# Kernel optimization log

Hardware: AMD Instinct MI355X
Metric: run time of the kernel (lower is better)

## Reference

```python
import jax, jax.numpy as jnp
import numpy as np

D = 2048      # model dim
H = 16        # query heads
KV = 4        # kv heads (GQA)
HD = 128      # head dim
L = 128       # latent dim (must equal HD for the residual add in the original module)
B = 2
S = 2048
ROPE_THETA = 10000.0


def _rope_cos_sin(seq_len, hd, start_pos, dtype):
    inv_freq = 1.0 / (ROPE_THETA ** (jnp.arange(0, hd, 2, dtype=jnp.float32) / hd))
    pos = jnp.arange(seq_len, dtype=jnp.float32) + start_pos
    freqs = pos[:, None] * inv_freq[None, :]          # [S, HD/2]
    emb = jnp.concatenate([freqs, freqs], axis=-1)    # [S, HD]
    return jnp.cos(emb).astype(dtype), jnp.sin(emb).astype(dtype)


def _rotate_half(x):
    h = x.shape[-1] // 2
    return jnp.concatenate([-x[..., h:], x[..., :h]], axis=-1)


def setup_inputs() -> dict:
    key = jax.random.key(0)
    ks = jax.random.split(key, 8)
    std = D ** -0.5
    x = jax.random.normal(ks[0], (B, S, D), dtype=jnp.float32)
    # causal mask [B, 1, S, S], 1 = keep, 0 = masked
    causal = jnp.tril(jnp.ones((S, S), dtype=jnp.int32))
    mask = jnp.broadcast_to(causal[None, None], (B, 1, S, S))
    # weights stored as [in, out] (== torch Linear weight transposed)
    wq = jax.random.normal(ks[1], (D, H * HD), dtype=jnp.float32) * std
    wk = jax.random.normal(ks[2], (D, KV * HD), dtype=jnp.float32) * std
    wv = jax.random.normal(ks[3], (D, KV * HD), dtype=jnp.float32) * std
    w_ql = jax.random.normal(ks[4], (D, L), dtype=jnp.float32) * std
    w_kl = jax.random.normal(ks[5], (D, L), dtype=jnp.float32) * std
    wo = jax.random.normal(ks[6], (H * HD, D), dtype=jnp.float32) * std
    return {"x": x, "mask": mask, "wq": wq, "wk": wk, "wv": wv,
            "w_ql": w_ql, "w_kl": w_kl, "wo": wo, "start_pos": 0}


def reference(x, mask, wq, wk, wv, w_ql, w_kl, wo, start_pos):
    b, s, _ = x.shape
    q = (x @ wq).reshape(b, s, H, HD)
    k = (x @ wk).reshape(b, s, KV, HD)
    v = (x @ wv).reshape(b, s, KV, HD)
    q_latent = x @ w_ql                               # [B,S,L]
    kv_latent = x @ w_kl                              # [B,S,L]

    cos, sin = _rope_cos_sin(s, HD, start_pos, x.dtype)
    c = cos[None, :, None, :]
    sn = sin[None, :, None, :]
    q = q * c + _rotate_half(q) * sn
    k = k * c + _rotate_half(k) * sn

    q = q.transpose(0, 2, 1, 3)                       # [B,H,S,HD]
    k = k.transpose(0, 2, 1, 3)                       # [B,KV,S,HD]
    v = v.transpose(0, 2, 1, 3)
    rep = H // KV
    k = jnp.repeat(k, rep, axis=1)                    # GQA repeat_interleave -> [B,H,S,HD]
    v = jnp.repeat(v, rep, axis=1)

    scores = jnp.einsum('bhqd,bhkd->bhqk', q, k) * (HD ** -0.5)
    scores = jnp.where(mask == 0, -jnp.inf, scores)
    attn = jax.nn.softmax(scores, axis=-1)
    out = jnp.einsum('bhqk,bhkd->bhqd', attn, v)
    out = out.transpose(0, 2, 1, 3).reshape(b, s, H * HD)

    latent_scores = jnp.einsum('bqd,bkd->bqk', q_latent, kv_latent) * (L ** -0.5)
    latent_scores = jnp.where(jnp.squeeze(mask, axis=1) == 0, -jnp.inf, latent_scores)
    latent_w = jax.nn.softmax(latent_scores, axis=-1)
    latent_out = jnp.einsum('bqk,bkd->bqd', latent_w, kv_latent)   # [B,S,L]

    # faithful to torch: unsqueeze(1).expand(B,H,S,L).contiguous().view(B,S,H*L)
    latent_exp = jnp.broadcast_to(latent_out[:, None], (b, H, s, L)).reshape(b, s, H * L)
    combined = out + latent_exp
    return combined @ wo
```

## Files before the change

kernel.cpp:

```cpp
#include <hip/hip_runtime.h>
#include <hip/hip_bf16.h>

typedef __bf16 bf16x8 __attribute__((ext_vector_type(8)));
typedef float f32x4 __attribute__((ext_vector_type(4)));
typedef unsigned short u16;

__device__ __forceinline__ float b2f(u16 u) {
  union { unsigned int i; float f; } v; v.i = ((unsigned int)u) << 16; return v.f;
}
__device__ __forceinline__ u16 f2b(float f) {
  union { float f; unsigned int i; } v; v.f = f;
  unsigned int r = v.i + 0x7fffu + ((v.i >> 16) & 1u);
  return (u16)(r >> 16);
}
__device__ __forceinline__ void gld_lds16(const u16* g, u16* l) {
  __builtin_amdgcn_global_load_lds(
      (const __attribute__((address_space(1))) unsigned int*)g,
      (__attribute__((address_space(3))) unsigned int*)l, 16, 0, 0);
}

#define NPROJ 3328

__global__ __launch_bounds__(256) void cvt_x(const float* __restrict__ x, u16* __restrict__ xb) {
  int i = (blockIdx.x * 256 + threadIdx.x) * 4;
  float4 v = *(const float4*)(x + i);
  u16 o[4] = { f2b(v.x), f2b(v.y), f2b(v.z), f2b(v.w) };
  *(uint2*)(xb + i) = *(uint2*)o;
}

__global__ __launch_bounds__(256) void prep_wt1(
    const float* __restrict__ wq, const float* __restrict__ wk, const float* __restrict__ wv,
    const float* __restrict__ wql, const float* __restrict__ wkl, u16* __restrict__ wt1) {
  __shared__ u16 lds[64][80];
  int bn = blockIdx.x % 52, bk = blockIdx.x / 52;
  int n0 = bn * 64, k0 = bk * 64;
  const float* src; int srcN, c0;
  if (n0 < 2048)      { src = wq;  srcN = 2048; c0 = n0; }
  else if (n0 < 2560) { src = wk;  srcN = 512;  c0 = n0 - 2048; }
  else if (n0 < 3072) { src = wv;  srcN = 512;  c0 = n0 - 2560; }
  else if (n0 < 3200) { src = wql; srcN = 128;  c0 = n0 - 3072; }
  else                { src = wkl; srcN = 128;  c0 = n0 - 3200; }
  int t = threadIdx.x;
  int row = t >> 2, cg = (t & 3) * 16;
  const float* p = src + (size_t)(k0 + row) * srcN + c0 + cg;
  u16 tmp[16];
#pragma unroll
  for (int g = 0; g < 4; ++g) {
    float4 v = *(const float4*)(p + g * 4);
    tmp[g*4+0] = f2b(v.x); tmp[g*4+1] = f2b(v.y);
    tmp[g*4+2] = f2b(v.z); tmp[g*4+3] = f2b(v.w);
  }
  *(uint4*)&lds[row][cg]     = *(uint4*)&tmp[0];
  *(uint4*)&lds[row][cg + 8] = *(uint4*)&tmp[8];
  __syncthreads();
  int n = t >> 2, kg = (t & 3) * 16;
  u16 ov[16];
#pragma unroll
  for (int i = 0; i < 16; ++i) ov[i] = lds[kg + i][n];
  u16* dst = wt1 + (size_t)(n0 + n) * 2048 + k0 + kg;
  *(uint4*)&dst[0] = *(uint4*)&ov[0];
  *(uint4*)&dst[8] = *(uint4*)&ov[8];
}

__global__ __launch_bounds__(256) void prep_wt2(const float* __restrict__ wo, u16* __restrict__ wt2) {
  __shared__ u16 lds[64][80];
  int bn = blockIdx.x & 31, bk = blockIdx.x >> 5;
  int n0 = bn * 64, k0 = bk * 64;
  int t = threadIdx.x;
  int row = t >> 2, cg = (t & 3) * 16;
  const float* p = wo + (size_t)(k0 + row) * 2048 + n0 + cg;
  u16 tmp[16];
#pragma unroll
  for (int g = 0; g < 4; ++g) {
    float4 v = *(const float4*)(p + g * 4);
    tmp[g*4+0] = f2b(v.x); tmp[g*4+1] = f2b(v.y);
    tmp[g*4+2] = f2b(v.z); tmp[g*4+3] = f2b(v.w);
  }
  *(uint4*)&lds[row][cg]     = *(uint4*)&tmp[0];
  *(uint4*)&lds[row][cg + 8] = *(uint4*)&tmp[8];
  __syncthreads();
  int n = t >> 2, kg = (t & 3) * 16;
  u16 ov[16];
#pragma unroll
  for (int i = 0; i < 16; ++i) ov[i] = lds[kg + i][n];
  u16* dst = wt2 + (size_t)(n0 + n) * 2048 + k0 + kg;
  *(uint4*)&dst[0] = *(uint4*)&ov[0];
  *(uint4*)&dst[8] = *(uint4*)&ov[8];
}

__global__ __launch_bounds__(256) void rope_table(float2* __restrict__ cs) {
  int idx = blockIdx.x * 256 + threadIdx.x;
  int p = idx >> 6, i = idx & 63;
  float invf = exp2f(-(float)i * 0.20762050593046938f);
  float a = (float)p * invf;
  cs[idx] = make_float2(cosf(a), sinf(a));
}

__global__ __launch_bounds__(256) void gemm_bf16(
    const u16* __restrict__ A, const u16* __restrict__ Bt, u16* __restrict__ C,
    float* __restrict__ Cf,
    int K, int lda, int ldb, int ldc, int nbn, const u16* __restrict__ lat) {
  __shared__ u16 As[128 * 64];
  __shared__ u16 Bs[128 * 64];
  int bm = blockIdx.x / nbn, bn = blockIdx.x % nbn;
  int m0 = bm * 128, n0 = bn * 128;
  int t = threadIdx.x;
  int lane = t & 63, wave = t >> 6;
  int wm = (wave >> 1) * 64, wn = (wave & 1) * 64;
  int lr = lane & 15, lg = lane >> 4;
  f32x4 acc[4][4] = {};
  for (int kt = 0; kt < K; kt += 64) {
    __syncthreads();
#pragma unroll
    for (int p = 0; p < 4; ++p) {
      int c = (p * 4 + wave) * 64 + lane;
      int row = c >> 3, col = (c & 7) * 8;
      gld_lds16(A + (size_t)(m0 + row) * lda + kt + col, As + c * 8);
      gld_lds16(Bt + (size_t)(n0 + row) * ldb + kt + col, Bs + c * 8);
    }
    __syncthreads();
#pragma unroll
    for (int ks = 0; ks < 2; ++ks) {
      bf16x8 af[4], bj[4];
#pragma unroll
      for (int i = 0; i < 4; ++i)
        af[i] = *(const bf16x8*)(As + (wm + i * 16 + lr) * 64 + ks * 32 + lg * 8);
#pragma unroll
      for (int j = 0; j < 4; ++j)
        bj[j] = *(const bf16x8*)(Bs + (wn + j * 16 + lr) * 64 + ks * 32 + lg * 8);
#pragma unroll
      for (int i = 0; i < 4; ++i)
#pragma unroll
        for (int j = 0; j < 4; ++j)
          acc[i][j] = __builtin_amdgcn_mfma_f32_16x16x32_bf16(af[i], bj[j], acc[i][j], 0, 0, 0);
    }
  }
#pragma unroll
  for (int i = 0; i < 4; ++i)
#pragma unroll
    for (int j = 0; j < 4; ++j)
#pragma unroll
      for (int r = 0; r < 4; ++r) {
        int mm = m0 + wm + i * 16 + lg * 4 + r;
        int nn = n0 + wn + j * 16 + lr;
        float v = acc[i][j][r];
        if (lat) {
          int b = mm >> 11, s2 = mm & 2047;
          v += b2f(lat[(size_t)(b * 128 + (s2 & 127)) * 2048 + nn]);
        }
        if (Cf) Cf[(size_t)mm * ldc + nn] = v;
        else    C [(size_t)mm * ldc + nn] = f2b(v);
      }
}

__global__ __launch_bounds__(256) void rope_kernel(u16* __restrict__ proj, const float2* __restrict__ cs) {
  int row = blockIdx.x;
  int s = row & 2047;
  const float2* csrow = cs + (size_t)s * 64;
  u16* prow = proj + (size_t)row * NPROJ;
  for (int u = threadIdx.x; u < 1280; u += 256) {
    int h = u >> 6, i = u & 63;
    int base = h * 128 + i;
    float2 c = csrow[i];
    float a = b2f(prow[base]), b = b2f(prow[base + 64]);
    prow[base]      = f2b(a * c.x - b * c.y);
    prow[base + 64] = f2b(b * c.x + a * c.y);
  }
}

__global__ __launch_bounds__(256) void transpose_v(const u16* __restrict__ proj,
                                                   u16* __restrict__ vt, u16* __restrict__ klt) {
  __shared__ u16 lds[64][80];
  int bid = blockIdx.x;
  int b = bid / 320, r = bid % 320;
  int ct = r / 32, st = r % 32;
  int c0 = ct < 8 ? 2560 + ct * 64 : 3200 + (ct - 8) * 64;
  int s0 = st * 64;
  int t = threadIdx.x;
  int srow = t >> 2, cg = (t & 3) * 16;
  const u16* p = proj + (size_t)(b * 2048 + s0 + srow) * NPROJ + c0 + cg;
  *(uint4*)&lds[srow][cg]     = *(const uint4*)p;
  *(uint4*)&lds[srow][cg + 8] = *(const uint4*)(p + 8);
  __syncthreads();
  int c = c0 + (t >> 2);
  int sg = (t & 3) * 16;
  u16 ov[16];
#pragma unroll
  for (int i = 0; i < 16; ++i) ov[i] = lds[sg + i][t >> 2];
  u16* dst;
  if (c < 3072) { int kv = (c - 2560) >> 7, d = (c - 2560) & 127;
                  dst = vt + ((size_t)(b * 4 + kv) * 128 + d) * 2048 + s0 + sg; }
  else          { int l = c - 3200;
                  dst = klt + (size_t)(b * 128 + l) * 2048 + s0 + sg; }
  *(uint4*)&dst[0] = *(uint4*)&ov[0];
  *(uint4*)&dst[8] = *(uint4*)&ov[8];
}

__global__ __launch_bounds__(256) void flash_attn(const u16* __restrict__ proj,
                                                  const u16* __restrict__ vt,
                                                  const u16* __restrict__ klt,
                                                  u16* __restrict__ acomb,
                                                  u16* __restrict__ latent) {
  __shared__ u16 Ks[64 * 136];
  __shared__ u16 Vs[128 * 72];
  __shared__ u16 Ps[4][16 * 72];
  int bid = blockIdx.x;
  int qt = bid & 31;
  int hh = (bid >> 5) % 17;
  int b  = bid / 544;
  int lane = threadIdx.x & 63, wave = threadIdx.x >> 6;
  int lr = lane & 15, lg = lane >> 4;

  int qcol = hh < 16 ? hh * 128 : 3072;
  int kcol = hh < 16 ? 2048 + (hh >> 2) * 128 : 3200;
  const u16* vsrc = hh < 16 ? vt + (size_t)(b * 4 + (hh >> 2)) * 128 * 2048
                            : klt + (size_t)b * 128 * 2048;

  int qbase = qt * 64 + wave * 16;
  const u16* qp = proj + (size_t)(b * 2048 + qbase) * NPROJ + qcol;
  bf16x8 aq[4];
#pragma unroll
  for (int ks = 0; ks < 4; ++ks)
    aq[ks] = *(const bf16x8*)(qp + (size_t)lr * NPROJ + ks * 32 + lg * 8);

  f32x4 o[8] = {};
  float m2[4]   = {-1e30f, -1e30f, -1e30f, -1e30f};
  float lsum[4] = {0.f, 0.f, 0.f, 0.f};
  const float scl = 0.08838834764831845f * 1.4426950408889634f;

  for (int kt = 0; kt <= qt; ++kt) {
    __syncthreads();
    {
      const u16* kg = proj + (size_t)(b * 2048 + kt * 64) * NPROJ + kcol;
#pragma unroll
      for (int p = 0; p < 4; ++p) {
        int c = p * 256 + threadIdx.x;
        int row = c >> 4, ch = c & 15;
        *(uint4*)(Ks + row * 136 + ch * 8) = *(const uint4*)(kg + (size_t)row * NPROJ + ch * 8);
      }
      const u16* vg = vsrc + kt * 64;
#pragma unroll
      for (int p = 0; p < 4; ++p) {
        int c = p * 256 + threadIdx.x;
        int row = c >> 3, ch = c & 7;
        *(uint4*)(Vs + row * 72 + ch * 8) = *(const uint4*)(vg + (size_t)row * 2048 + ch * 8);
      }
    }
    __syncthreads();

    f32x4 sv[4];
#pragma unroll
    for (int fr = 0; fr < 4; ++fr) {
      f32x4 a = {};
      int key = fr * 16 + lr;
#pragma unroll
      for (int ks = 0; ks < 4; ++ks) {
        bf16x8 bk = *(const bf16x8*)(Ks + key * 136 + ks * 32 + lg * 8);
        a = __builtin_amdgcn_mfma_f32_16x16x32_bf16(aq[ks], bk, a, 0, 0, 0);
      }
      sv[fr] = a;
    }
#pragma unroll
    for (int fr = 0; fr < 4; ++fr) {
      int key = kt * 64 + fr * 16 + lr;
#pragma unroll
      for (int r = 0; r < 4; ++r) {
        int q = qbase + lg * 4 + r;
        sv[fr][r] = (key <= q) ? sv[fr][r] * scl : -1e30f;
      }
    }
#pragma unroll
    for (int r = 0; r < 4; ++r) {
      float mx = fmaxf(fmaxf(sv[0][r], sv[1][r]), fmaxf(sv[2][r], sv[3][r]));
      mx = fmaxf(mx, __shfl_xor(mx, 1));
      mx = fmaxf(mx, __shfl_xor(mx, 2));
      mx = fmaxf(mx, __shfl_xor(mx, 4));
      mx = fmaxf(mx, __shfl_xor(mx, 8));
      float mn = fmaxf(m2[r], mx);
      float corr = exp2f(m2[r] - mn);
      m2[r] = mn;
      float rs = 0.f;
#pragma unroll
      for (int fr = 0; fr < 4; ++fr) {
        float pp = exp2f(sv[fr][r] - mn);
        sv[fr][r] = pp;
        rs += pp;
      }
      rs += __shfl_xor(rs, 1); rs += __shfl_xor(rs, 2);
      rs += __shfl_xor(rs, 4); rs += __shfl_xor(rs, 8);
      lsum[r] = lsum[r] * corr + rs;
#pragma unroll
      for (int cf = 0; cf < 8; ++cf) o[cf][r] *= corr;
    }
    u16* ps = &Ps[wave][0];
#pragma unroll
    for (int fr = 0; fr < 4; ++fr)
#pragma unroll
      for (int r = 0; r < 4; ++r) {
        int q = lg * 4 + r;
        int key = fr * 16 + lr;
        ps[q * 72 + key] = f2b(sv[fr][r]);
      }
#pragma unroll
    for (int ks = 0; ks < 2; ++ks) {
      bf16x8 ap = *(const bf16x8*)(ps + lr * 72 + ks * 32 + lg * 8);
#pragma unroll
      for (int cf = 0; cf < 8; ++cf) {
        int d = cf * 16 + lr;
        bf16x8 bv = *(const bf16x8*)(Vs + d * 72 + ks * 32 + lg * 8);
        o[cf] = __builtin_amdgcn_mfma_f32_16x16x32_bf16(ap, bv, o[cf], 0, 0, 0);
      }
    }
  }
  u16* obase; size_t ostride;
  if (hh < 16) { obase = acomb + hh * 128; ostride = 2048; }
  else         { obase = latent;           ostride = 128; }
#pragma unroll
  for (int r = 0; r < 4; ++r) {
    float inv = 1.0f / lsum[r];
    int q = qbase + lg * 4 + r;
    u16* orow = obase + (size_t)(b * 2048 + q) * ostride;
#pragma unroll
    for (int cf = 0; cf < 8; ++cf)
      orow[cf * 16 + lr] = f2b(o[cf][r] * inv);
  }
}

extern "C" void kernel_launch(void* const* d_in, const int* in_sizes, int n_in,
                              void* d_out, int out_size, void* d_ws, size_t ws_size,
                              hipStream_t stream) {
  const float* x   = (const float*)d_in[0];
  const float* wq  = (const float*)d_in[2];
  const float* wk  = (const float*)d_in[3];
  const float* wv  = (const float*)d_in[4];
  const float* wql = (const float*)d_in[5];
  const float* wkl = (const float*)d_in[6];
  const float* wo  = (const float*)d_in[7];

  char* ws = (char*)d_ws;
  u16*    proj  = (u16*)(ws + 0);
  u16*    wt2   = (u16*)(ws + 0);
  u16*    wt1   = (u16*)(ws + 27262976);
  float2* cs    = (float2*)(ws + 27262976);
  u16*    vt    = (u16*)(ws + 28311552);
  u16*    klt   = (u16*)(ws + 32505856);
  u16*    latent= (u16*)(ws + 33554432);
  u16*    lout  = (u16*)(ws + 34603008);
  u16*    xb    = (u16*)(ws + 40894464);
  u16*    acomb = (u16*)(ws + 40894464);
  float*  out   = (float*)d_out;

  prep_wt1<<<52 * 32, 256, 0, stream>>>(wq, wk, wv, wql, wkl, wt1);
  cvt_x<<<8192, 256, 0, stream>>>(x, xb);
  gemm_bf16<<<32 * 26, 256, 0, stream>>>(xb, wt1, proj, nullptr, 2048, 2048, 2048, NPROJ, 26, nullptr);
  rope_table<<<512, 256, 0, stream>>>(cs);
  rope_kernel<<<4096, 256, 0, stream>>>(proj, cs);
  transpose_v<<<640, 256, 0, stream>>>(proj, vt, klt);
  flash_attn<<<2 * 17 * 32, 256, 0, stream>>>(proj, vt, klt, acomb, latent);
  prep_wt2<<<32 * 32, 256, 0, stream>>>(wo, wt2);
  gemm_bf16<<<2 * 16, 256, 0, stream>>>(latent, wt2, lout, nullptr, 2048, 2048, 2048, 2048, 16, nullptr);
  gemm_bf16<<<32 * 16, 256, 0, stream>>>(acomb, wt2, nullptr, out, 2048, 2048, 2048, 2048, 16, lout);
}
```

Baseline: 671.6 us.

## Read K/V fragments directly from global memory and schedule longest query tiles first

The flash attention kernel no longer stages K and V tiles through shared memory with block-wide barriers. Each wave now loads its MFMA operands straight from global memory and relies on the cache for reuse across the four waves. The grid is also remapped so blocks with the most causal work (the largest query tile index) launch first, padding each row to 40 blocks with early exits. This trades LDS traffic and syncs for redundant, less coalesced global loads, since each wave fetches the same K/V data.

```diff
diff --git a/kernel.cpp b/kernel.cpp
--- a/kernel.cpp
+++ b/kernel.cpp
@@ -201,13 +201,13 @@
                                                   const u16* __restrict__ klt,
                                                   u16* __restrict__ acomb,
                                                   u16* __restrict__ latent) {
-  __shared__ u16 Ks[64 * 136];
-  __shared__ u16 Vs[128 * 72];
   __shared__ u16 Ps[4][16 * 72];
   int bid = blockIdx.x;
-  int qt = bid & 31;
-  int hh = (bid >> 5) % 17;
-  int b  = bid / 544;
+  int g = bid % 40;
+  if (g >= 34) return;
+  int qt = 31 - bid / 40;
+  int hh = g % 17;
+  int b  = g / 17;
   int lane = threadIdx.x & 63, wave = threadIdx.x >> 6;
   int lr = lane & 15, lg = lane >> 4;
 
@@ -223,39 +223,23 @@
   for (int ks = 0; ks < 4; ++ks)
     aq[ks] = *(const bf16x8*)(qp + (size_t)lr * NPROJ + ks * 32 + lg * 8);
 
+  const u16* kbase = proj + (size_t)(b * 2048) * NPROJ + kcol;
+
   f32x4 o[8] = {};
   float m2[4]   = {-1e30f, -1e30f, -1e30f, -1e30f};
   float lsum[4] = {0.f, 0.f, 0.f, 0.f};
   const float scl = 0.08838834764831845f * 1.4426950408889634f;
 
   for (int kt = 0; kt <= qt; ++kt) {
-    __syncthreads();
-    {
-      const u16* kg = proj + (size_t)(b * 2048 + kt * 64) * NPROJ + kcol;
-#pragma unroll
-      for (int p = 0; p < 4; ++p) {
-        int c = p * 256 + threadIdx.x;
-        int row = c >> 4, ch = c & 15;
-        *(uint4*)(Ks + row * 136 + ch * 8) = *(const uint4*)(kg + (size_t)row * NPROJ + ch * 8);
-      }
-      const u16* vg = vsrc + kt * 64;
-#pragma unroll
-      for (int p = 0; p < 4; ++p) {
-        int c = p * 256 + threadIdx.x;
-        int row = c >> 3, ch = c & 7;
-        *(uint4*)(Vs + row * 72 + ch * 8) = *(const uint4*)(vg + (size_t)row * 2048 + ch * 8);
-      }
-    }
-    __syncthreads();
-
+    const u16* kg = kbase + (size_t)(kt * 64) * NPROJ;
     f32x4 sv[4];
 #pragma unroll
     for (int fr = 0; fr < 4; ++fr) {
       f32x4 a = {};
-      int key = fr * 16 + lr;
+      const u16* krow = kg + (size_t)(fr * 16 + lr) * NPROJ + lg * 8;
 #pragma unroll
       for (int ks = 0; ks < 4; ++ks) {
-        bf16x8 bk = *(const bf16x8*)(Ks + key * 136 + ks * 32 + lg * 8);
+        bf16x8 bk = *(const bf16x8*)(krow + ks * 32);
         a = __builtin_amdgcn_mfma_f32_16x16x32_bf16(aq[ks], bk, a, 0, 0, 0);
       }
       sv[fr] = a;
@@ -301,13 +285,13 @@
         int key = fr * 16 + lr;
         ps[q * 72 + key] = f2b(sv[fr][r]);
       }
+    const u16* vg = vsrc + kt * 64 + lg * 8;
 #pragma unroll
     for (int ks = 0; ks < 2; ++ks) {
       bf16x8 ap = *(const bf16x8*)(ps + lr * 72 + ks * 32 + lg * 8);
 #pragma unroll
       for (int cf = 0; cf < 8; ++cf) {
-        int d = cf * 16 + lr;
-        bf16x8 bv = *(const bf16x8*)(Vs + d * 72 + ks * 32 + lg * 8);
+        bf16x8 bv = *(const bf16x8*)(vg + (size_t)(cf * 16 + lr) * 2048 + ks * 32);
         o[cf] = __builtin_amdgcn_mfma_f32_16x16x32_bf16(ap, bv, o[cf], 0, 0, 0);
       }
     }
@@ -356,7 +340,7 @@
   rope_table<<<512, 256, 0, stream>>>(cs);
   rope_kernel<<<4096, 256, 0, stream>>>(proj, cs);
   transpose_v<<<640, 256, 0, stream>>>(proj, vt, klt);
-  flash_attn<<<2 * 17 * 32, 256, 0, stream>>>(proj, vt, klt, acomb, latent);
+  flash_attn<<<40 * 32, 256, 0, stream>>>(proj, vt, klt, acomb, latent);
   prep_wt2<<<32 * 32, 256, 0, stream>>>(wo, wt2);
   gemm_bf16<<<2 * 16, 256, 0, stream>>>(latent, wt2, lout, nullptr, 2048, 2048, 2048, 2048, 16, nullptr);
   gemm_bf16<<<32 * 16, 256, 0, stream>>>(acomb, wt2, nullptr, out, 2048, 2048, 2048, 2048, 16, lout);
```

Measured after the change: 688.1 us. 1.02x slower.
